# Performance work log

Hardware: AMD Instinct MI355X
Metric: run time of the kernel (lower is better)

Reference implementation:

```python
import jax, jax.numpy as jnp
import numpy as np

N = 50000
E = 800000
IN_DIM = 128
HID = 64
NUM_LAYERS = 3


def setup_inputs() -> dict:
    key = jax.random.key(0)
    k1, k2, k3, k4, k5 = jax.random.split(key, 5)
    x = jax.random.normal(k1, (N, IN_DIM), dtype=jnp.float32)
    edge_index = jax.random.randint(k2, (2, E), 0, N, dtype=jnp.int64)
    # xemb linear: in_channels -> hidden_channels (PyTorch default init scale)
    lim = 1.0 / np.sqrt(IN_DIM)
    W = jax.random.uniform(k3, (IN_DIM, HID), minval=-lim, maxval=lim, dtype=jnp.float32)
    b = jax.random.uniform(k4, (HID,), minval=-lim, maxval=lim, dtype=jnp.float32)
    return {"x": x, "edge_index": edge_index, "W": W, "b": b}


def _pure_gcn_conv(x, row, col, norm):
    # norm = rsqrt(1 + deg), deg = row-sum of adjacency
    x = norm * x                                            # [N, H]
    agg = jax.ops.segment_sum(x[col], row, num_segments=N)  # spmm_add(adj_t, x)
    return norm * (agg + x)


def reference(x, edge_index, W, b):
    row, col = edge_index[0], edge_index[1]
    # degree = adj_t.sum(dim=-1): count of edges per row
    deg = jax.ops.segment_sum(jnp.ones((E,), dtype=x.dtype), row, num_segments=N)
    norm = jax.lax.rsqrt(1.0 + deg)[:, None]  # [N, 1]
    # xemb: Dropout(0) -> Linear -> Identity
    h = x @ W + b  # [N, HID]
    for _ in range(NUM_LAYERS):
        h = _pure_gcn_conv(h, row, col, norm)
    return h
```

## Files before the change

### kernel.cpp

```cpp
#include <hip/hip_runtime.h>
#include <hip/hip_fp16.h>

#define IN_DIM 128
#define HID 64
#define XPAD 132
#define EPB 4096
#define MAXNB 512
#define BCAP 3072


__global__ __launch_bounds__(512) void zero_kernel(int* __restrict__ p, int n) {
    int i = threadIdx.x;
    if (i < n) p[i] = 0;
}

__global__ __launch_bounds__(256) void bucket_fill_kernel(
        const int* __restrict__ rows, const int* __restrict__ cols,
        int* __restrict__ gcursor, int* __restrict__ pairs, int E, int NB) {
    __shared__ int cnt[MAXNB];
    __shared__ int bas[MAXNB];
    for (int i = threadIdx.x; i < NB; i += 256) cnt[i] = 0;
    __syncthreads();
    int base = blockIdx.x * EPB;
    int m = E - base; if (m > EPB) m = EPB;
    int r[16], c[16];
    #pragma unroll
    for (int u = 0; u < 16; ++u) {
        int k = u * 256 + threadIdx.x;
        r[u] = -1;
        if (k < m) {
            r[u] = rows[base + k];
            c[u] = cols[base + k];
            atomicAdd(&cnt[r[u] >> 7], 1);
        }
    }
    __syncthreads();
    for (int i = threadIdx.x; i < NB; i += 256) {
        int cc = cnt[i];
        bas[i] = cc ? atomicAdd(&gcursor[i], cc) : 0;
        cnt[i] = 0;
    }
    __syncthreads();
    #pragma unroll
    for (int u = 0; u < 16; ++u) {
        if (r[u] >= 0) {
            int bkt = r[u] >> 7;
            int pos = bas[bkt] + atomicAdd(&cnt[bkt], 1);
            pairs[bkt * BCAP + pos] = ((r[u] & 127) << 16) | c[u];
        }
    }
}

__global__ __launch_bounds__(256) void bucket_sort_kernel(
        const int* __restrict__ pairs, const int* __restrict__ gcursor,
        int2* __restrict__ row_range, int* __restrict__ col_sorted,
        float* __restrict__ norm, int N) {
    __shared__ int cnt[128];
    __shared__ int scan[128];
    const int t = threadIdx.x;
    const int r0 = blockIdx.x << 7;
    const int pb = blockIdx.x * BCAP;
    const int m = gcursor[blockIdx.x];

    if (t < 128) cnt[t] = 0;
    __syncthreads();
    for (int k = t; k < m; k += 256)
        atomicAdd(&cnt[pairs[pb + k] >> 16], 1);
    __syncthreads();

    int v = (t < 128) ? cnt[t] : 0;
    if (t < 128) scan[t] = v;
    __syncthreads();
    #pragma unroll
    for (int off = 1; off < 128; off <<= 1) {
        int tmp = (t < 128 && t >= off) ? scan[t - off] : 0;
        __syncthreads();
        if (t < 128) scan[t] += tmp;
        __syncthreads();
    }
    if (t < 128) {
        int ex = scan[t] - v;
        int rr = r0 + t;
        if (rr < N) {
            row_range[rr] = make_int2(pb + ex, pb + ex + v);
            norm[rr]      = rsqrtf(1.0f + (float)v);
        }
        cnt[t] = ex;
    }
    __syncthreads();
    for (int k = t; k < m; k += 256) {
        int p = pairs[pb + k];
        int pos = pb + atomicAdd(&cnt[p >> 16], 1);
        col_sorted[pos] = p & 0xFFFF;
    }
}


__global__ __launch_bounds__(256) void linear_kernel(
        const float* __restrict__ x, const float* __restrict__ W,
        const float* __restrict__ b, const float* __restrict__ norm,
        uint2* __restrict__ xs, int N) {
    __shared__ float xl[64 * XPAD];
    const int tid = threadIdx.x;
    const int row0 = blockIdx.x * 64;

    for (int idx = tid; idx < 64 * (IN_DIM / 4); idx += 256) {
        int r = idx >> 5;
        int c4 = idx & 31;
        int gr = row0 + r;
        float4 v = make_float4(0.f, 0.f, 0.f, 0.f);
        if (gr < N) v = reinterpret_cast<const float4*>(x)[(size_t)gr * 32 + c4];
        *reinterpret_cast<float4*>(&xl[r * XPAD + c4 * 4]) = v;
    }
    __syncthreads();

    const int c4 = tid & 15;
    const int rg = tid >> 4;
    const float4 bv = reinterpret_cast<const float4*>(b)[c4];
    float4 acc[4];
    #pragma unroll
    for (int rr = 0; rr < 4; ++rr) acc[rr] = bv;

    const float4* Wv = reinterpret_cast<const float4*>(W);
    for (int k0 = 0; k0 < IN_DIM; k0 += 4) {
        float4 w0 = Wv[(k0 + 0) * 16 + c4];
        float4 w1 = Wv[(k0 + 1) * 16 + c4];
        float4 w2 = Wv[(k0 + 2) * 16 + c4];
        float4 w3 = Wv[(k0 + 3) * 16 + c4];
        #pragma unroll
        for (int rr = 0; rr < 4; ++rr) {
            float4 xv = *reinterpret_cast<const float4*>(&xl[(rg * 4 + rr) * XPAD + k0]);
            acc[rr].x = fmaf(xv.x, w0.x, acc[rr].x);
            acc[rr].y = fmaf(xv.x, w0.y, acc[rr].y);
            acc[rr].z = fmaf(xv.x, w0.z, acc[rr].z);
            acc[rr].w = fmaf(xv.x, w0.w, acc[rr].w);
            acc[rr].x = fmaf(xv.y, w1.x, acc[rr].x);
            acc[rr].y = fmaf(xv.y, w1.y, acc[rr].y);
            acc[rr].z = fmaf(xv.y, w1.z, acc[rr].z);
            acc[rr].w = fmaf(xv.y, w1.w, acc[rr].w);
            acc[rr].x = fmaf(xv.z, w2.x, acc[rr].x);
            acc[rr].y = fmaf(xv.z, w2.y, acc[rr].y);
            acc[rr].z = fmaf(xv.z, w2.z, acc[rr].z);
            acc[rr].w = fmaf(xv.z, w2.w, acc[rr].w);
            acc[rr].x = fmaf(xv.w, w3.x, acc[rr].x);
            acc[rr].y = fmaf(xv.w, w3.y, acc[rr].y);
            acc[rr].z = fmaf(xv.w, w3.z, acc[rr].z);
            acc[rr].w = fmaf(xv.w, w3.w, acc[rr].w);
        }
    }

    #pragma unroll
    for (int rr = 0; rr < 4; ++rr) {
        int gr = row0 + rg * 4 + rr;
        if (gr >= N) continue;
        float nv = norm[gr];
        __half2 h0 = __floats2half2_rn(nv * acc[rr].x, nv * acc[rr].y);
        __half2 h1 = __floats2half2_rn(nv * acc[rr].z, nv * acc[rr].w);
        uint2 pk;
        pk.x = *reinterpret_cast<unsigned int*>(&h0);
        pk.y = *reinterpret_cast<unsigned int*>(&h1);
        xs[(size_t)gr * 16 + c4] = pk;
    }
}


__global__ __launch_bounds__(256) void layer_kernel(
        const int2* __restrict__ row_range, const int* __restrict__ col_sorted,
        const uint2* __restrict__ xin, const float* __restrict__ norm,
        void* __restrict__ xout_v, int N, int last) {
    int node = (blockIdx.x * blockDim.x + threadIdx.x) >> 6;
    int lane = threadIdx.x & 63;
    if (node >= N) return;
    const int f = lane & 15;
    const int g = lane >> 4;

    int2 rr = row_range[node];
    int be = rr.x;
    int en = rr.y;
    float ax = 0.f, ay = 0.f, az = 0.f, aw = 0.f;

    for (int base = be; base < en; base += 64) {
        int m = en - base;
        if (m > 64) m = 64;
        int cv = (lane < m) ? col_sorted[base + lane] : 0;
        int t = 0;
        for (; t + 16 <= m; t += 16) {
            int c0 = __shfl(cv, t + 0 + g, 64);
            int c1 = __shfl(cv, t + 4 + g, 64);
            int c2 = __shfl(cv, t + 8 + g, 64);
            int c3 = __shfl(cv, t + 12 + g, 64);
            uint2 u0 = xin[(size_t)c0 * 16 + f];
            uint2 u1 = xin[(size_t)c1 * 16 + f];
            uint2 u2 = xin[(size_t)c2 * 16 + f];
            uint2 u3 = xin[(size_t)c3 * 16 + f];
            float2 p0 = __half22float2(*reinterpret_cast<__half2*>(&u0.x));
            float2 q0 = __half22float2(*reinterpret_cast<__half2*>(&u0.y));
            float2 p1 = __half22float2(*reinterpret_cast<__half2*>(&u1.x));
            float2 q1 = __half22float2(*reinterpret_cast<__half2*>(&u1.y));
            float2 p2 = __half22float2(*reinterpret_cast<__half2*>(&u2.x));
            float2 q2 = __half22float2(*reinterpret_cast<__half2*>(&u2.y));
            float2 p3 = __half22float2(*reinterpret_cast<__half2*>(&u3.x));
            float2 q3 = __half22float2(*reinterpret_cast<__half2*>(&u3.y));
            ax += (p0.x + p1.x) + (p2.x + p3.x);
            ay += (p0.y + p1.y) + (p2.y + p3.y);
            az += (q0.x + q1.x) + (q2.x + q3.x);
            aw += (q0.y + q1.y) + (q2.y + q3.y);
        }
        for (; t + 4 <= m; t += 4) {
            int c = __shfl(cv, t + g, 64);
            uint2 u = xin[(size_t)c * 16 + f];
            float2 p = __half22float2(*reinterpret_cast<__half2*>(&u.x));
            float2 q = __half22float2(*reinterpret_cast<__half2*>(&u.y));
            ax += p.x; ay += p.y; az += q.x; aw += q.y;
        }
        int rem = m - t;
        if (rem > 0) {
            int c = __shfl(cv, t + g, 64);
            if (g < rem) {
                uint2 u = xin[(size_t)c * 16 + f];
                float2 p = __half22float2(*reinterpret_cast<__half2*>(&u.x));
                float2 q = __half22float2(*reinterpret_cast<__half2*>(&u.y));
                ax += p.x; ay += p.y; az += q.x; aw += q.y;
            }
        }
    }

    ax += __shfl_xor(ax, 16, 64); ax += __shfl_xor(ax, 32, 64);
    ay += __shfl_xor(ay, 16, 64); ay += __shfl_xor(ay, 32, 64);
    az += __shfl_xor(az, 16, 64); az += __shfl_xor(az, 32, 64);
    aw += __shfl_xor(aw, 16, 64); aw += __shfl_xor(aw, 32, 64);

    uint2 us = xin[(size_t)node * 16 + f];
    float2 sp = __half22float2(*reinterpret_cast<__half2*>(&us.x));
    float2 sq = __half22float2(*reinterpret_cast<__half2*>(&us.y));
    float nv = norm[node];
    float hx = nv * (ax + sp.x);
    float hy = nv * (ay + sp.y);
    float hz = nv * (az + sq.x);
    float hw = nv * (aw + sq.y);
    if (g == 0) {
        if (last) {
            reinterpret_cast<float4*>(xout_v)[(size_t)node * 16 + f] =
                make_float4(hx, hy, hz, hw);
        } else {
            __half2 o0 = __floats2half2_rn(nv * hx, nv * hy);
            __half2 o1 = __floats2half2_rn(nv * hz, nv * hw);
            uint2 pk;
            pk.x = *reinterpret_cast<unsigned int*>(&o0);
            pk.y = *reinterpret_cast<unsigned int*>(&o1);
            reinterpret_cast<uint2*>(xout_v)[(size_t)node * 16 + f] = pk;
        }
    }
}

extern "C" void kernel_launch(void* const* d_in, const int* in_sizes, int n_in,
                              void* d_out, int out_size, void* d_ws, size_t ws_size,
                              hipStream_t stream) {
    const float* x  = (const float*)d_in[0];
    const int*   ei = (const int*)d_in[1];
    const float* W  = (const float*)d_in[2];
    const float* b  = (const float*)d_in[3];
    float* out = (float*)d_out;

    const int N = in_sizes[0] / IN_DIM;
    const int E = in_sizes[1] / 2;
    const int* rows = ei;
    const int* cols = ei + E;
    const int NB = (N + 127) >> 7;

    char* wp = (char*)d_ws;
    auto alloc = [&](size_t bytes) {
        char* r = wp;
        wp += (bytes + 15) & ~(size_t)15;
        return r;
    };
    int*   pairs      = (int*)alloc((size_t)NB * BCAP * sizeof(int));
    int*   col_sorted = (int*)alloc((size_t)NB * BCAP * sizeof(int));
    int*   gcursor    = (int*)alloc(MAXNB * sizeof(int));
    int2*  row_range  = (int2*)alloc((size_t)N * sizeof(int2));
    float* norm       = (float*)alloc((size_t)N * sizeof(float));
    uint2* xsA        = (uint2*)alloc((size_t)N * 16 * sizeof(uint2));
    uint2* xsB        = (uint2*)alloc((size_t)N * 16 * sizeof(uint2));

    const int eblocks = (E + EPB - 1) / EPB;

    zero_kernel<<<1, 512, 0, stream>>>(gcursor, MAXNB);
    bucket_fill_kernel<<<eblocks, 256, 0, stream>>>(rows, cols, gcursor, pairs, E, NB);
    bucket_sort_kernel<<<NB, 256, 0, stream>>>(pairs, gcursor, row_range, col_sorted, norm, N);

    linear_kernel<<<(N + 63) / 64, 256, 0, stream>>>(x, W, b, norm, xsA, N);

    const int blocks = (N * 64 + 255) / 256;
    layer_kernel<<<blocks, 256, 0, stream>>>(row_range, col_sorted, xsA, norm, xsB, N, 0);
    layer_kernel<<<blocks, 256, 0, stream>>>(row_range, col_sorted, xsB, norm, xsA, N, 0);
    layer_kernel<<<blocks, 256, 0, stream>>>(row_range, col_sorted, xsA, norm, out, N, 1);
}
```

Baseline: 127.3 us.

## Fuse bucket sort with linear embedding and sort columns within each row

Merges the per-bucket CSR sort kernel and the linear projection kernel into one launch, so each block handles both the 128 rows of its bucket and their linear transform. Norm values are taken from shared memory instead of being reloaded from global memory. Columns are first staged in shared memory and insertion-sorted within each row, which gives the later gathers better locality. The cost is fewer, heavier blocks for the GEMM part (about 391 instead of about 782), serial insertion sorts done by one thread per row, and more shared memory per block.

```diff
diff --git a/kernel.cpp b/kernel.cpp
--- a/kernel.cpp
+++ b/kernel.cpp
@@ -51,16 +51,24 @@
     }
 }
 
-__global__ __launch_bounds__(256) void bucket_sort_kernel(
+
+__global__ __launch_bounds__(256) void sort_linear_kernel(
         const int* __restrict__ pairs, const int* __restrict__ gcursor,
+        const float* __restrict__ x, const float* __restrict__ W,
+        const float* __restrict__ bias,
         int2* __restrict__ row_range, int* __restrict__ col_sorted,
-        float* __restrict__ norm, int N) {
+        float* __restrict__ norm_g, uint2* __restrict__ xs, int N) {
+    __shared__ float xl[64 * XPAD];
     __shared__ int cnt[128];
-    __shared__ int scan[128];
+    __shared__ int scan_s[128];
+    __shared__ float nrm[128];
+    int* colbuf = (int*)xl;
+
     const int t = threadIdx.x;
-    const int r0 = blockIdx.x << 7;
-    const int pb = blockIdx.x * BCAP;
-    const int m = gcursor[blockIdx.x];
+    const int bkt = blockIdx.x;
+    const int r0 = bkt << 7;
+    const int pb = bkt * BCAP;
+    const int m = gcursor[bkt];
 
     if (t < 128) cnt[t] = 0;
     __syncthreads();
@@ -69,97 +77,106 @@
     __syncthreads();
 
     int v = (t < 128) ? cnt[t] : 0;
-    if (t < 128) scan[t] = v;
+    if (t < 128) scan_s[t] = v;
     __syncthreads();
     #pragma unroll
     for (int off = 1; off < 128; off <<= 1) {
-        int tmp = (t < 128 && t >= off) ? scan[t - off] : 0;
+        int tmp = (t < 128 && t >= off) ? scan_s[t - off] : 0;
         __syncthreads();
-        if (t < 128) scan[t] += tmp;
+        if (t < 128) scan_s[t] += tmp;
         __syncthreads();
     }
+    int ex = 0;
     if (t < 128) {
-        int ex = scan[t] - v;
+        ex = scan_s[t] - v;
         int rr = r0 + t;
+        float nv = rsqrtf(1.0f + (float)v);
+        nrm[t] = nv;
         if (rr < N) {
             row_range[rr] = make_int2(pb + ex, pb + ex + v);
-            norm[rr]      = rsqrtf(1.0f + (float)v);
+            norm_g[rr]    = nv;
         }
         cnt[t] = ex;
     }
     __syncthreads();
     for (int k = t; k < m; k += 256) {
         int p = pairs[pb + k];
-        int pos = pb + atomicAdd(&cnt[p >> 16], 1);
-        col_sorted[pos] = p & 0xFFFF;
-    }
-}
-
-
-__global__ __launch_bounds__(256) void linear_kernel(
-        const float* __restrict__ x, const float* __restrict__ W,
-        const float* __restrict__ b, const float* __restrict__ norm,
-        uint2* __restrict__ xs, int N) {
-    __shared__ float xl[64 * XPAD];
-    const int tid = threadIdx.x;
-    const int row0 = blockIdx.x * 64;
-
-    for (int idx = tid; idx < 64 * (IN_DIM / 4); idx += 256) {
-        int r = idx >> 5;
-        int c4 = idx & 31;
-        int gr = row0 + r;
-        float4 v = make_float4(0.f, 0.f, 0.f, 0.f);
-        if (gr < N) v = reinterpret_cast<const float4*>(x)[(size_t)gr * 32 + c4];
-        *reinterpret_cast<float4*>(&xl[r * XPAD + c4 * 4]) = v;
-    }
-    __syncthreads();
-
-    const int c4 = tid & 15;
-    const int rg = tid >> 4;
-    const float4 bv = reinterpret_cast<const float4*>(b)[c4];
-    float4 acc[4];
-    #pragma unroll
-    for (int rr = 0; rr < 4; ++rr) acc[rr] = bv;
-
+        int pos = atomicAdd(&cnt[p >> 16], 1);
+        colbuf[pos] = p & 0xFFFF;
+    }
+    __syncthreads();
+    if (t < 128) {
+        for (int i = ex + 1; i < ex + v; ++i) {
+            int key = colbuf[i];
+            int j = i - 1;
+            while (j >= ex && colbuf[j] > key) { colbuf[j + 1] = colbuf[j]; --j; }
+            colbuf[j + 1] = key;
+        }
+    }
+    __syncthreads();
+    for (int k = t; k < m; k += 256)
+        col_sorted[pb + k] = colbuf[k];
+
+    const int c4 = t & 15;
+    const int rg = t >> 4;
+    const float4 bv = reinterpret_cast<const float4*>(bias)[c4];
     const float4* Wv = reinterpret_cast<const float4*>(W);
-    for (int k0 = 0; k0 < IN_DIM; k0 += 4) {
-        float4 w0 = Wv[(k0 + 0) * 16 + c4];
-        float4 w1 = Wv[(k0 + 1) * 16 + c4];
-        float4 w2 = Wv[(k0 + 2) * 16 + c4];
-        float4 w3 = Wv[(k0 + 3) * 16 + c4];
+
+    for (int half = 0; half < 2; ++half) {
+        const int hrow0 = r0 + half * 64;
+        __syncthreads();
+        for (int idx = t; idx < 64 * 32; idx += 256) {
+            int r = idx >> 5, cc = idx & 31;
+            int gr = hrow0 + r;
+            float4 vv = make_float4(0.f, 0.f, 0.f, 0.f);
+            if (gr < N) vv = reinterpret_cast<const float4*>(x)[(size_t)gr * 32 + cc];
+            *reinterpret_cast<float4*>(&xl[r * XPAD + cc * 4]) = vv;
+        }
+        __syncthreads();
+
+        float4 acc[4];
+        #pragma unroll
+        for (int rr = 0; rr < 4; ++rr) acc[rr] = bv;
+        for (int k0 = 0; k0 < IN_DIM; k0 += 4) {
+            float4 w0 = Wv[(k0 + 0) * 16 + c4];
+            float4 w1 = Wv[(k0 + 1) * 16 + c4];
+            float4 w2 = Wv[(k0 + 2) * 16 + c4];
+            float4 w3 = Wv[(k0 + 3) * 16 + c4];
+            #pragma unroll
+            for (int rr = 0; rr < 4; ++rr) {
+                float4 xv = *reinterpret_cast<const float4*>(&xl[(rg * 4 + rr) * XPAD + k0]);
+                acc[rr].x = fmaf(xv.x, w0.x, acc[rr].x);
+                acc[rr].y = fmaf(xv.x, w0.y, acc[rr].y);
+                acc[rr].z = fmaf(xv.x, w0.z, acc[rr].z);
+                acc[rr].w = fmaf(xv.x, w0.w, acc[rr].w);
+                acc[rr].x = fmaf(xv.y, w1.x, acc[rr].x);
+                acc[rr].y = fmaf(xv.y, w1.y, acc[rr].y);
+                acc[rr].z = fmaf(xv.y, w1.z, acc[rr].z);
+                acc[rr].w = fmaf(xv.y, w1.w, acc[rr].w);
+                acc[rr].x = fmaf(xv.z, w2.x, acc[rr].x);
+                acc[rr].y = fmaf(xv.z, w2.y, acc[rr].y);
+                acc[rr].z = fmaf(xv.z, w2.z, acc[rr].z);
+                acc[rr].w = fmaf(xv.z, w2.w, acc[rr].w);
+                acc[rr].x = fmaf(xv.w, w3.x, acc[rr].x);
+                acc[rr].y = fmaf(xv.w, w3.y, acc[rr].y);
+                acc[rr].z = fmaf(xv.w, w3.z, acc[rr].z);
+                acc[rr].w = fmaf(xv.w, w3.w, acc[rr].w);
+            }
+        }
+
         #pragma unroll
         for (int rr = 0; rr < 4; ++rr) {
-            float4 xv = *reinterpret_cast<const float4*>(&xl[(rg * 4 + rr) * XPAD + k0]);
-            acc[rr].x = fmaf(xv.x, w0.x, acc[rr].x);
-            acc[rr].y = fmaf(xv.x, w0.y, acc[rr].y);
-            acc[rr].z = fmaf(xv.x, w0.z, acc[rr].z);
-            acc[rr].w = fmaf(xv.x, w0.w, acc[rr].w);
-            acc[rr].x = fmaf(xv.y, w1.x, acc[rr].x);
-            acc[rr].y = fmaf(xv.y, w1.y, acc[rr].y);
-            acc[rr].z = fmaf(xv.y, w1.z, acc[rr].z);
-            acc[rr].w = fmaf(xv.y, w1.w, acc[rr].w);
-            acc[rr].x = fmaf(xv.z, w2.x, acc[rr].x);
-            acc[rr].y = fmaf(xv.z, w2.y, acc[rr].y);
-            acc[rr].z = fmaf(xv.z, w2.z, acc[rr].z);
-            acc[rr].w = fmaf(xv.z, w2.w, acc[rr].w);
-            acc[rr].x = fmaf(xv.w, w3.x, acc[rr].x);
-            acc[rr].y = fmaf(xv.w, w3.y, acc[rr].y);
-            acc[rr].z = fmaf(xv.w, w3.z, acc[rr].z);
-            acc[rr].w = fmaf(xv.w, w3.w, acc[rr].w);
-        }
-    }
-
-    #pragma unroll
-    for (int rr = 0; rr < 4; ++rr) {
-        int gr = row0 + rg * 4 + rr;
-        if (gr >= N) continue;
-        float nv = norm[gr];
-        __half2 h0 = __floats2half2_rn(nv * acc[rr].x, nv * acc[rr].y);
-        __half2 h1 = __floats2half2_rn(nv * acc[rr].z, nv * acc[rr].w);
-        uint2 pk;
-        pk.x = *reinterpret_cast<unsigned int*>(&h0);
-        pk.y = *reinterpret_cast<unsigned int*>(&h1);
-        xs[(size_t)gr * 16 + c4] = pk;
+            int lr = rg * 4 + rr;
+            int gr = hrow0 + lr;
+            if (gr >= N) continue;
+            float nv = nrm[half * 64 + lr];
+            __half2 h0 = __floats2half2_rn(nv * acc[rr].x, nv * acc[rr].y);
+            __half2 h1 = __floats2half2_rn(nv * acc[rr].z, nv * acc[rr].w);
+            uint2 pk;
+            pk.x = *reinterpret_cast<unsigned int*>(&h0);
+            pk.y = *reinterpret_cast<unsigned int*>(&h1);
+            xs[(size_t)gr * 16 + c4] = pk;
+        }
     }
 }
 
@@ -286,9 +303,8 @@
 
     zero_kernel<<<1, 512, 0, stream>>>(gcursor, MAXNB);
     bucket_fill_kernel<<<eblocks, 256, 0, stream>>>(rows, cols, gcursor, pairs, E, NB);
-    bucket_sort_kernel<<<NB, 256, 0, stream>>>(pairs, gcursor, row_range, col_sorted, norm, N);
-
-    linear_kernel<<<(N + 63) / 64, 256, 0, stream>>>(x, W, b, norm, xsA, N);
+    sort_linear_kernel<<<NB, 256, 0, stream>>>(pairs, gcursor, x, W, b,
+                                               row_range, col_sorted, norm, xsA, N);
 
     const int blocks = (N * 64 + 255) / 256;
     layer_kernel<<<blocks, 256, 0, stream>>>(row_range, col_sorted, xsA, norm, xsB, N, 0);
```

Result: slower. 156.7 us (+23.1%).
